# Performance work log

Hardware: AMD Instinct MI355X
Metric: run time of the kernel (lower is better)

The kernel has to match this reference:

```python
import jax, jax.numpy as jnp
import numpy as np

B_, L_, DM = 2, 2048, 1024
DS, DC, EXP, HD = 128, 4, 2, 64
DI = EXP * DM              # 2048
NH = DI // HD              # 32 heads
CONV_DIM = DI + 2 * DS     # 2304
DIN = 2 * DI + 2 * DS + NH # 4384 (z, xBC, dt)
CS = 256                   # SSD chunk size
EPS = 1e-5


def setup_inputs() -> dict:
    key = jax.random.key(0)
    ks = jax.random.split(key, 8)
    s = 0.02
    x = jax.random.normal(ks[0], (B_, L_, DM), jnp.float32)
    norm_w = jnp.ones((DM,), jnp.float32)
    in_proj_w = jax.random.normal(ks[1], (DIN, DM), jnp.float32) * s
    conv_w = jax.random.normal(ks[2], (CONV_DIM, DC), jnp.float32) * 0.2
    conv_b = jnp.zeros((CONV_DIM,), jnp.float32)
    # inverse-softplus of dt ~ U(0.001, 0.1)
    dt_bias = jnp.log(jnp.expm1(jax.random.uniform(ks[3], (NH,), minval=0.001, maxval=0.1)))
    A_log = jnp.log(jax.random.uniform(ks[4], (NH,), minval=1.0, maxval=16.0))
    D = jnp.ones((NH,), jnp.float32)
    gnorm_w = jnp.ones((DI,), jnp.float32)
    out_proj_w = jax.random.normal(ks[5], (DM, DI), jnp.float32) * s
    return dict(x=x, norm_w=norm_w, in_proj_w=in_proj_w, conv_w=conv_w, conv_b=conv_b,
                dt_bias=dt_bias, A_log=A_log, D=D, gnorm_w=gnorm_w, out_proj_w=out_proj_w)


def _segsum(a):
    # a: [..., T] -> [..., T, T]; (i,j) = sum_{j<k<=i} a_k, -inf above diagonal
    T = a.shape[-1]
    cs = jnp.cumsum(a, -1)
    seg = cs[..., :, None] - cs[..., None, :]
    mask = jnp.tril(jnp.ones((T, T), bool))
    return jnp.where(mask, seg, -jnp.inf)


def _ssd(X, A, Bm, Cm):
    # X: [b,l,h,p] (= x*dt), A: [b,l,h] (= dt*a), Bm,Cm: [b,l,n] (ngroups=1)
    b, l, h, p = X.shape
    n, nc = Bm.shape[-1], l // CS
    X = X.reshape(b, nc, CS, h, p)
    A = A.reshape(b, nc, CS, h).transpose(0, 3, 1, 2)  # [b,h,c,s]
    Bm = Bm.reshape(b, nc, CS, n)
    Cm = Cm.reshape(b, nc, CS, n)
    Acs = jnp.cumsum(A, -1)                            # [b,h,c,s]
    Lmat = jnp.exp(_segsum(A))                         # [b,h,c,s,s]
    Y_diag = jnp.einsum('bcln,bcsn,bhcls,bcshp->bclhp', Cm, Bm, Lmat, X)
    decay_states = jnp.exp(Acs[..., -1:] - Acs)        # [b,h,c,s]
    states = jnp.einsum('bcln,bhcl,bclhp->bchpn', Bm, decay_states, X)
    states = jnp.concatenate([jnp.zeros_like(states[:, :1]), states], axis=1)  # [b,c+1,h,p,n]
    decay_chunk = jnp.exp(_segsum(jnp.pad(Acs[..., -1], ((0, 0), (0, 0), (1, 0)))))  # [b,h,c+1,c+1]
    states = jnp.einsum('bhzc,bchpn->bzhpn', decay_chunk, states)[:, :-1]
    Y_off = jnp.einsum('bcln,bchpn,bhcl->bclhp', Cm, states, jnp.exp(Acs))
    return (Y_diag + Y_off).reshape(b, l, h, p)


def _forward(x, norm_w, in_proj_w, conv_w, conv_b, dt_bias, A_log, D, gnorm_w, out_proj_w):
    b, l, _ = x.shape
    # outer RMSNorm
    xn = x * jax.lax.rsqrt(jnp.mean(x * x, -1, keepdims=True) + EPS) * norm_w
    zxbcdt = jnp.einsum('bld,ed->ble', xn, in_proj_w)
    z = zxbcdt[..., :DI]
    xBC = zxbcdt[..., DI:DI + CONV_DIM]
    dt = zxbcdt[..., -NH:]
    # causal depthwise conv1d + bias + silu
    pad = jnp.pad(xBC, ((0, 0), (DC - 1, 0), (0, 0)))
    conv = sum(pad[:, k:k + l, :] * conv_w[:, k] for k in range(DC)) + conv_b
    xBC = conv * jax.nn.sigmoid(conv)
    xs = xBC[..., :DI]
    Bm = xBC[..., DI:DI + DS]
    Cm = xBC[..., DI + DS:]
    dt = jax.nn.softplus(dt + dt_bias)                 # [b,l,h]
    A = -jnp.exp(A_log)                                # [h]
    xh = xs.reshape(b, l, NH, HD)
    y = _ssd(xh * dt[..., None], dt * A, Bm, Cm)
    y = y + D[None, None, :, None] * xh
    y = y.reshape(b, l, DI)
    # gated RMSNorm (norm_before_gate=False): rmsnorm(y * silu(z)) * w
    y = y * (z * jax.nn.sigmoid(z))
    y = y * jax.lax.rsqrt(jnp.mean(y * y, -1, keepdims=True) + EPS) * gnorm_w
    return x + jnp.einsum('bld,ed->ble', y, out_proj_w)


def reference(x, norm_w, in_proj_w, conv_w, conv_b, dt_bias, A_log, D, gnorm_w, out_proj_w):
    return _forward(x, norm_w, in_proj_w, conv_w, conv_b, dt_bias, A_log, D, gnorm_w, out_proj_w)
```

## Files before the change

### kernel.cpp

```cpp
#include <hip/hip_runtime.h>
#include <hip/hip_bf16.h>

#define BB      2
#define LSEQ    2048
#define DMODEL  1024
#define DSTATE  128
#define DCONV   4
#define HEADDIM 64
#define DINNER  2048
#define NHEADS  32
#define CONVD   2304
#define DINP    4384
#define CHUNK   256
#define NCH     8
#define NROWS   4096
#define EPSF    1e-5f
#define TPAD    264
#define WIPAD   4480

typedef __attribute__((ext_vector_type(8))) short bf16x8;
typedef __attribute__((ext_vector_type(4))) float f32x4;

#define ASYNC_COPY16(gptr, lptr) \
    __builtin_amdgcn_global_load_lds((const __attribute__((address_space(1))) void*)(gptr), \
                                     (__attribute__((address_space(3))) void*)(lptr), 16, 0, 0)

__device__ __forceinline__ ushort f2bf(float f) {
    __hip_bfloat16 h = __float2bfloat16(f);
    return *(ushort*)&h;
}
__device__ __forceinline__ float bf2f(ushort u) {
    return __uint_as_float(((unsigned)u) << 16);
}
__device__ __forceinline__ short fb(float f) { return (short)f2bf(f); }
__device__ __forceinline__ short tb(float f) { return (short)(__float_as_uint(f) >> 16); }

__global__ __launch_bounds__(256) void prologue_kernel(
    const float* __restrict__ x, const float* __restrict__ norm_w,
    const float* __restrict__ in_proj_w, const float* __restrict__ out_proj_w,
    const float* __restrict__ gnorm_w,
    ushort* __restrict__ xn_bf, ushort* __restrict__ wi_bf,
    ushort* __restrict__ wo_bf, float* __restrict__ ssq)
{
    int bid = blockIdx.x;
    if (bid < 4480) {
        long i4 = ((long)bid * 256 + threadIdx.x) * 4;
        int n = (int)(i4 >> 10);
        long k = i4 & 1023;
        ushort4 o;
        if (n < DINP) {
            float4 v = *(const float4*)(in_proj_w + ((long)n << 10) + k);
            o.x = f2bf(v.x); o.y = f2bf(v.y); o.z = f2bf(v.z); o.w = f2bf(v.w);
        } else { o.x = o.y = o.z = o.w = 0; }
        *(ushort4*)(wi_bf + i4) = o;
    } else if (bid < 6528) {
        long i4 = ((long)(bid - 4480) * 256 + threadIdx.x) * 4;
        int k = (int)(i4 & 2047);
        float4 v = *(const float4*)(out_proj_w + i4);
        float4 g = *(const float4*)(gnorm_w + k);
        ushort4 o;
        o.x = f2bf(v.x * g.x); o.y = f2bf(v.y * g.y);
        o.z = f2bf(v.z * g.z); o.w = f2bf(v.w * g.w);
        *(ushort4*)(wo_bf + i4) = o;
    } else if (bid < 10624) {
        int row = bid - 6528;
        const float* xr = x + (long)row * DMODEL;
        float4 v = *(const float4*)(xr + threadIdx.x * 4);
        float ss = v.x*v.x + v.y*v.y + v.z*v.z + v.w*v.w;
        for (int off = 32; off; off >>= 1) ss += __shfl_down(ss, off, 64);
        __shared__ float red[4];
        if ((threadIdx.x & 63) == 0) red[threadIdx.x >> 6] = ss;
        __syncthreads();
        float tot = red[0] + red[1] + red[2] + red[3];
        float scale = rsqrtf(tot / (float)DMODEL + EPSF);
        float4 wv = *(const float4*)(norm_w + threadIdx.x * 4);
        ushort4 o;
        o.x = f2bf(v.x * scale * wv.x); o.y = f2bf(v.y * scale * wv.y);
        o.z = f2bf(v.z * scale * wv.z); o.w = f2bf(v.w * scale * wv.w);
        *(ushort4*)(xn_bf + (long)row * DMODEL + threadIdx.x * 4) = o;
    } else {
        ssq[(bid - 10624) * 256 + threadIdx.x] = 0.f;
    }
}

__global__ __launch_bounds__(256, 3) void gemm_bf16_kernel(
    const ushort* __restrict__ A, int lda, long sA,
    const ushort* __restrict__ W, int ldw, long sW,
    void* __restrict__ Cout, int ldc, long sC, int c_bf16,
    const float* __restrict__ resid, const float* __restrict__ rowscale,
    int mtiles, int ntiles, int N, int K)
{
    __shared__ __align__(16) char smem[34816];
    ushort* As = (ushort*)smem;
    ushort* Bs = As + 128 * 64;
    ushort* tu = (ushort*)smem;
    float*  tf = (float*)smem;

    const int t = threadIdx.x;
    const int lane = t & 63;
    const int w = t >> 6;
    const int wm = w & 1, wn = w >> 1;
    const int lm = lane & 15, quad = lane >> 4;

    int pid = blockIdx.x;
    const int GM = 8;
    int width = GM * ntiles;
    int group = pid / width;
    int first_m = group * GM;
    int gsz = mtiles - first_m; if (gsz > GM) gsz = GM;
    int mt = first_m + (pid % width) % gsz;
    int nt = (pid % width) / gsz;
    const int m0 = mt * 128, n0 = nt * 128;

    A += (long)blockIdx.z * sA;
    W += (long)blockIdx.z * sW;

    const ushort* ga[4]; const ushort* gw[4];
#pragma unroll
    for (int i = 0; i < 4; ++i) {
        int s = i * 256 + t;
        int row = s >> 3;
        int kseg = (s & 7) ^ (row & 7);
        ga[i] = A + (long)(m0 + row) * lda + kseg * 8;
        gw[i] = W + (long)(n0 + row) * ldw + kseg * 8;
    }

    f32x4 acc[4][4];
    f32x4 zero4 = {0.f, 0.f, 0.f, 0.f};
#pragma unroll
    for (int i = 0; i < 4; ++i)
#pragma unroll
        for (int j = 0; j < 4; ++j) acc[i][j] = zero4;

    int arow8[4], arow7[4], brow8[4], brow7[4];
#pragma unroll
    for (int i = 0; i < 4; ++i) {
        int ar = wm * 64 + i * 16 + lm;
        arow8[i] = ar * 8; arow7[i] = ar & 7;
        int br = wn * 64 + i * 16 + lm;
        brow8[i] = br * 8; brow7[i] = br & 7;
    }

    for (int k0 = 0; k0 < K; k0 += 64) {
#pragma unroll
        for (int i = 0; i < 4; ++i) {
            ASYNC_COPY16(ga[i], &As[(i * 256 + w * 64) * 8]);
            ga[i] += 64;
        }
#pragma unroll
        for (int i = 0; i < 4; ++i) {
            ASYNC_COPY16(gw[i], &Bs[(i * 256 + w * 64) * 8]);
            gw[i] += 64;
        }
        __syncthreads();
#pragma unroll
        for (int ks = 0; ks < 2; ++ks) {
            bf16x8 af[4], bfr[4];
#pragma unroll
            for (int i = 0; i < 4; ++i)
                af[i]  = *(const bf16x8*)&As[(arow8[i] + ((ks * 4 + quad) ^ arow7[i])) * 8];
#pragma unroll
            for (int i = 0; i < 4; ++i)
                bfr[i] = *(const bf16x8*)&Bs[(brow8[i] + ((ks * 4 + quad) ^ brow7[i])) * 8];
#pragma unroll
            for (int im = 0; im < 4; ++im)
#pragma unroll
                for (int in = 0; in < 4; ++in)
                    acc[im][in] = __builtin_amdgcn_mfma_f32_16x16x32_bf16(
                        af[im], bfr[in], acc[im][in], 0, 0, 0);
        }
        __syncthreads();
    }

    if (c_bf16) {
        ushort* C = (ushort*)Cout + (long)blockIdx.z * sC;
#pragma unroll
        for (int mi = 0; mi < 4; ++mi)
#pragma unroll
            for (int ni = 0; ni < 4; ++ni) {
                int c = wn * 64 + ni * 16 + lm;
#pragma unroll
                for (int i = 0; i < 4; ++i) {
                    int r = wm * 64 + mi * 16 + quad * 4 + i;
                    tu[r * 136 + c] = f2bf(acc[mi][ni][i]);
                }
            }
        __syncthreads();
        int r = t >> 1, cb = (t & 1) * 64;
        long rowbase = (long)(m0 + r) * ldc + n0 + cb;
#pragma unroll
        for (int q = 0; q < 8; ++q) {
            int gcol = n0 + cb + q * 8;
            if (gcol < N)
                *(bf16x8*)(C + rowbase + q * 8) =
                    *(const bf16x8*)&tu[r * 136 + cb + q * 8];
        }
    } else {
        float* C = (float*)Cout + (long)blockIdx.z * sC;
#pragma unroll
        for (int p = 0; p < 2; ++p) {
            if (wm == p) {
#pragma unroll
                for (int mi = 0; mi < 4; ++mi)
#pragma unroll
                    for (int i = 0; i < 4; ++i) {
                        int r = mi * 16 + quad * 4 + i;
                        float s = 1.f;
                        if (rowscale)
                            s = rsqrtf(rowscale[m0 + p * 64 + r] * (1.f / (float)DINNER) + EPSF);
#pragma unroll
                        for (int ni = 0; ni < 4; ++ni) {
                            int c = wn * 64 + ni * 16 + lm;
                            tf[r * 132 + c] = acc[mi][ni][i] * s;
                        }
                    }
            }
            __syncthreads();
            int r2 = t >> 2, cb = (t & 3) * 32;
            long gbase = (long)(m0 + p * 64 + r2) * ldc + n0 + cb;
#pragma unroll
            for (int q = 0; q < 8; ++q) {
                float4 v = *(const float4*)&tf[r2 * 132 + cb + q * 4];
                if (resid) {
                    float4 rv = *(const float4*)(resid + gbase + q * 4);
                    v.x += rv.x; v.y += rv.y; v.z += rv.z; v.w += rv.w;
                }
                *(float4*)(C + gbase + q * 4) = v;
            }
            __syncthreads();
        }
    }
}

__device__ __forceinline__ void conv8_row(
    const ushort* __restrict__ zx, const float* __restrict__ cw,
    const float* __restrict__ cb, ushort* __restrict__ xBC_bf,
    int row, int l, int c)
{
    float4 cwv[8];
#pragma unroll
    for (int j = 0; j < 8; ++j) cwv[j] = *(const float4*)(cw + (c + j) * 4);
    float acc[8];
    {
        float4 b0 = *(const float4*)(cb + c);
        float4 b1 = *(const float4*)(cb + c + 4);
        acc[0] = b0.x; acc[1] = b0.y; acc[2] = b0.z; acc[3] = b0.w;
        acc[4] = b1.x; acc[5] = b1.y; acc[6] = b1.z; acc[7] = b1.w;
    }
#pragma unroll
    for (int k = 0; k < DCONV; ++k) {
        int ls = l + k - (DCONV - 1);
        if (ls >= 0) {
            const ushort* zr = zx + (long)(row + k - (DCONV - 1)) * DINP + DINNER + c;
            ushort4 a = *(const ushort4*)zr;
            ushort4 b = *(const ushort4*)(zr + 4);
            acc[0] += bf2f(a.x) * ((const float*)&cwv[0])[k];
            acc[1] += bf2f(a.y) * ((const float*)&cwv[1])[k];
            acc[2] += bf2f(a.z) * ((const float*)&cwv[2])[k];
            acc[3] += bf2f(a.w) * ((const float*)&cwv[3])[k];
            acc[4] += bf2f(b.x) * ((const float*)&cwv[4])[k];
            acc[5] += bf2f(b.y) * ((const float*)&cwv[5])[k];
            acc[6] += bf2f(b.z) * ((const float*)&cwv[6])[k];
            acc[7] += bf2f(b.w) * ((const float*)&cwv[7])[k];
        }
    }
    ushort o[8];
#pragma unroll
    for (int j = 0; j < 8; ++j)
        o[j] = f2bf(acc[j] / (1.f + __expf(-acc[j])));
    ushort* dst = xBC_bf + (long)row * CONVD + c;
    *(ushort4*)dst = *(ushort4*)&o[0];
    *(ushort4*)(dst + 4) = *(ushort4*)&o[4];
}

__global__ __launch_bounds__(256) void conv_acs_kernel(
    const ushort* __restrict__ zx, const float* __restrict__ cw,
    const float* __restrict__ cb, ushort* __restrict__ xBC_bf,
    const float* __restrict__ dt_bias, const float* __restrict__ A_log,
    float* __restrict__ dtv, float* __restrict__ Acs)
{
    int bid = blockIdx.x;
    int t = threadIdx.x;
    if (bid < NROWS) {
        int row = bid;
        int l = row & (LSEQ - 1);
        conv8_row(zx, cw, cb, xBC_bf, row, l, t * 8);
        if (t < 32)
            conv8_row(zx, cw, cb, xBC_bf, row, l, 2048 + t * 8);
    } else {
        __shared__ float buf[2 * CHUNK];
        int idx = bid - NROWS;
        int bc = idx >> 5, h = idx & 31;
        int l = t;
        int row = bc * CHUNK + l;
        float v = bf2f(zx[(long)row * DINP + (DINP - NHEADS) + h]) + dt_bias[h];
        float d = (v > 20.f) ? v : log1pf(__expf(v));
        dtv[row * NHEADS + h] = d;
        float a = -d * __expf(A_log[h]);
        buf[l] = a; __syncthreads();
        int src = 0;
        for (int off = 1; off < CHUNK; off <<= 1) {
            float vv = buf[src * CHUNK + l];
            if (l >= off) vv += buf[src * CHUNK + l - off];
            buf[(src ^ 1) * CHUNK + l] = vv;
            __syncthreads();
            src ^= 1;
        }
        Acs[(bc * NHEADS + h) * CHUNK + l] = buf[src * CHUNK + l];
    }
}

__global__ __launch_bounds__(256) void prep_b_kernel(
    const ushort* __restrict__ xBC_bf, ushort* __restrict__ Bt)
{
    int bc = blockIdx.x, half = blockIdx.y;
    int t = threadIdx.x;
    int row0 = bc * CHUNK;
    __shared__ ushort tB[64 * TPAD];
    int src_c0 = DINNER + half * 64;
    for (int iter = 0; iter < 8; ++iter) {
        int l = iter * 32 + (t >> 3);
        int cc = (t & 7) * 8;
        ushort u[8];
        *(ushort4*)&u[0] = *(const ushort4*)(xBC_bf + (long)(row0 + l) * CONVD + src_c0 + cc);
        *(ushort4*)&u[4] = *(const ushort4*)(xBC_bf + (long)(row0 + l) * CONVD + src_c0 + cc + 4);
#pragma unroll
        for (int j = 0; j < 8; ++j) tB[(cc + j) * TPAD + l] = u[j];
    }
    __syncthreads();
    int r = t >> 2, seg = (t & 3) * 64;
    ushort* dst = Bt + ((long)bc * DSTATE + half * 64 + r) * CHUNK + seg;
    const ushort* s1 = &tB[r * TPAD + seg];
#pragma unroll
    for (int q = 0; q < 16; ++q)
        *(ushort4*)(dst + q * 4) = *(const ushort4*)(s1 + q * 4);
}

__global__ __launch_bounds__(256) void chunk_state_mfma_kernel(
    const ushort* __restrict__ xBC_bf, const ushort* __restrict__ Bt,
    const float* __restrict__ dtv, const float* __restrict__ acs,
    ushort* __restrict__ state)
{
    int bc = blockIdx.x, h = blockIdx.y;
    int t = threadIdx.x, lane = t & 63, w = t >> 6;
    int lm = lane & 15, quad = lane >> 4;
    int row0 = bc * CHUNK;
    __shared__ ushort xt[64 * TPAD];
    __shared__ float cl[CHUNK];
    {
        float a = acs[(bc * NHEADS + h) * CHUNK + t];
        float T = acs[(bc * NHEADS + h) * CHUNK + CHUNK - 1];
        cl[t] = __expf(T - a) * dtv[(row0 + t) * NHEADS + h];
    }
    __syncthreads();
    for (int iter = 0; iter < 8; ++iter) {
        int l = iter * 32 + (t >> 3);
        int cc = (t & 7) * 8;
        ushort u[8];
        *(ushort4*)&u[0] = *(const ushort4*)(xBC_bf + (long)(row0 + l) * CONVD + h * HEADDIM + cc);
        *(ushort4*)&u[4] = *(const ushort4*)(xBC_bf + (long)(row0 + l) * CONVD + h * HEADDIM + cc + 4);
        float sc = cl[l];
#pragma unroll
        for (int j = 0; j < 8; ++j)
            xt[(cc + j) * TPAD + l] = (ushort)tb(bf2f(u[j]) * sc);
    }
    __syncthreads();

    const ushort* Bb = Bt + (long)bc * DSTATE * CHUNK;
    f32x4 acc[4][2];
    f32x4 zero4 = {0.f, 0.f, 0.f, 0.f};
#pragma unroll
    for (int i = 0; i < 4; ++i) { acc[i][0] = zero4; acc[i][1] = zero4; }

    for (int kt = 0; kt < 8; ++kt) {
        int k = kt * 32 + quad * 8;
        bf16x8 af[4], bfr[2];
#pragma unroll
        for (int mi = 0; mi < 4; ++mi)
            af[mi] = *(const bf16x8*)&xt[(mi * 16 + lm) * TPAD + k];
#pragma unroll
        for (int nj = 0; nj < 2; ++nj)
            bfr[nj] = *(const bf16x8*)(Bb + (long)(w * 32 + nj * 16 + lm) * CHUNK + k);
#pragma unroll
        for (int mi = 0; mi < 4; ++mi)
#pragma unroll
            for (int nj = 0; nj < 2; ++nj)
                acc[mi][nj] = __builtin_amdgcn_mfma_f32_16x16x32_bf16(
                    af[mi], bfr[nj], acc[mi][nj], 0, 0, 0);
    }
    ushort* sp = state + (long)(bc * NHEADS + h) * (DSTATE * HEADDIM);
#pragma unroll
    for (int mi = 0; mi < 4; ++mi)
#pragma unroll
        for (int nj = 0; nj < 2; ++nj) {
            int n = w * 32 + nj * 16 + lm;
#pragma unroll
            for (int i = 0; i < 4; ++i) {
                int p = mi * 16 + quad * 4 + i;
                sp[p * DSTATE + n] = f2bf(acc[mi][nj][i]);
            }
        }
}

__global__ __launch_bounds__(256) void state_scan_kernel(
    ushort* __restrict__ state, const float* __restrict__ Acs)
{
    long flat = (long)blockIdx.x * 256 + threadIdx.x;
    int e = (int)(flat & 8191);
    int bh = (int)(flat >> 13);
    int b = bh >> 5, h = bh & 31;
    float S = 0.f;
    for (int c = 0; c < NCH; ++c) {
        int bc = b * NCH + c;
        long idx = ((long)(bc * NHEADS + h)) * 8192 + e;
        float T = Acs[(bc * NHEADS + h) * CHUNK + CHUNK - 1];
        float tmp = bf2f(state[idx]);
        state[idx] = f2bf(S);
        S = S * __expf(T) + tmp;
    }
}

__global__ __launch_bounds__(256) void ssd_y_mfma_kernel(
    const ushort* __restrict__ xBC_bf, const ushort* __restrict__ G2b,
    const float* __restrict__ acs, const ushort* __restrict__ state,
    const ushort* __restrict__ zxb, const float* __restrict__ dtv,
    const float* __restrict__ Dh, ushort* __restrict__ ybf,
    float* __restrict__ ssq)
{
    int bc = blockIdx.x, h = blockIdx.y;
    int t = threadIdx.x, lane = t & 63, w = t >> 6;
    int lm = lane & 15, quad = lane >> 4;
    int row0 = bc * CHUNK;
    __shared__ ushort xt[64 * TPAD];
    __shared__ float acs_s[CHUNK];
    __shared__ float dl[CHUNK];
    acs_s[t] = acs[(bc * NHEADS + h) * CHUNK + t];
    dl[t] = dtv[(row0 + t) * NHEADS + h];
    __syncthreads();
    for (int iter = 0; iter < 8; ++iter) {
        int l = iter * 32 + (t >> 3);
        int cc = (t & 7) * 8;
        ushort u[8];
        *(ushort4*)&u[0] = *(const ushort4*)(xBC_bf + (long)(row0 + l) * CONVD + h * HEADDIM + cc);
        *(ushort4*)&u[4] = *(const ushort4*)(xBC_bf + (long)(row0 + l) * CONVD + h * HEADDIM + cc + 4);
        float sd = dl[l];
#pragma unroll
        for (int j = 0; j < 8; ++j)
            xt[(cc + j) * TPAD + l] = (ushort)tb(bf2f(u[j]) * sd);
    }
    __syncthreads();

    int lbase = w * 64;
    float acs_l[4], eAl[4];
#pragma unroll
    for (int mi = 0; mi < 4; ++mi) {
        acs_l[mi] = acs_s[lbase + mi * 16 + lm];
        eAl[mi] = __expf(acs_l[mi]);
    }
    f32x4 acc[4][4];
    f32x4 zero4 = {0.f, 0.f, 0.f, 0.f};
#pragma unroll
    for (int i = 0; i < 4; ++i)
#pragma unroll
        for (int j = 0; j < 4; ++j) acc[i][j] = zero4;

    const ushort* g2 = G2b + (long)bc * (CHUNK * CHUNK);

    for (int ks = 0; ks <= 2 * w + 1; ++ks) {
        int sq = ks * 32 + quad * 8;
        bf16x8 bfr[4];
#pragma unroll
        for (int ni = 0; ni < 4; ++ni)
            bfr[ni] = *(const bf16x8*)&xt[(ni * 16 + lm) * TPAD + sq];
        float base = acs_s[sq];
        float e8[8];
        e8[0] = 1.f;
#pragma unroll
        for (int j = 1; j < 8; ++j)
            e8[j] = __expf(fminf(base - acs_s[sq + j], 80.f));
#pragma unroll
        for (int mi = 0; mi < 4; ++mi) {
            int lmin = lbase + mi * 16;
            if (ks * 32 > lmin + 15) continue;
            int lv = lmin + lm;
            float em = __expf(fminf(acs_l[mi] - base, 0.f));
            bf16x8 g8 = *(const bf16x8*)(g2 + (long)lv * CHUNK + sq);
            bf16x8 af;
#pragma unroll
            for (int j = 0; j < 8; ++j) {
                float v = bf2f((ushort)g8[j]) * (em * e8[j]);
                af[j] = (sq + j > lv) ? (short)0 : tb(v);
            }
#pragma unroll
            for (int ni = 0; ni < 4; ++ni)
                acc[mi][ni] = __builtin_amdgcn_mfma_f32_16x16x32_bf16(
                    af, bfr[ni], acc[mi][ni], 0, 0, 0);
        }
    }

    const ushort* sp = state + (long)(bc * NHEADS + h) * (DSTATE * HEADDIM);
    const ushort* Cb = xBC_bf + (long)row0 * CONVD + DINNER + DSTATE;
    for (int kt = 0; kt < 4; ++kt) {
        int n0 = kt * 32 + quad * 8;
        bf16x8 bfr[4];
#pragma unroll
        for (int ni = 0; ni < 4; ++ni)
            bfr[ni] = *(const bf16x8*)(sp + (long)(ni * 16 + lm) * DSTATE + n0);
#pragma unroll
        for (int mi = 0; mi < 4; ++mi) {
            int lv = lbase + mi * 16 + lm;
            bf16x8 cu = *(const bf16x8*)(Cb + (long)lv * CONVD + n0);
            bf16x8 ce;
            float e = eAl[mi];
#pragma unroll
            for (int j = 0; j < 8; ++j) ce[j] = tb(bf2f((ushort)cu[j]) * e);
#pragma unroll
            for (int ni = 0; ni < 4; ++ni)
                acc[mi][ni] = __builtin_amdgcn_mfma_f32_16x16x32_bf16(
                    ce, bfr[ni], acc[mi][ni], 0, 0, 0);
        }
    }

    float Dv = Dh[h];
#pragma unroll
    for (int mi = 0; mi < 4; ++mi)
#pragma unroll
        for (int i = 0; i < 4; ++i) {
            int l = lbase + mi * 16 + quad * 4 + i;
            long row = row0 + l;
            float ps = 0.f;
#pragma unroll
            for (int ni = 0; ni < 4; ++ni) {
                int p = ni * 16 + lm;
                float xh = bf2f(xBC_bf[row * CONVD + h * HEADDIM + p]);
                float z = bf2f(zxb[row * DINP + h * HEADDIM + p]);
                float o = (acc[mi][ni][i] + Dv * xh) * (z / (1.f + __expf(-z)));
                ps += o * o;
                ybf[row * DINNER + h * HEADDIM + p] = f2bf(o);
            }
#pragma unroll
            for (int m = 1; m < 16; m <<= 1) ps += __shfl_xor(ps, m, 64);
            if (lm == 0) atomicAdd(&ssq[row], ps);
        }
}

extern "C" void kernel_launch(void* const* d_in, const int* in_sizes, int n_in,
                              void* d_out, int out_size, void* d_ws, size_t ws_size,
                              hipStream_t stream)
{
    (void)in_sizes; (void)n_in; (void)out_size; (void)ws_size;
    const float* x          = (const float*)d_in[0];
    const float* norm_w     = (const float*)d_in[1];
    const float* in_proj_w  = (const float*)d_in[2];
    const float* conv_w     = (const float*)d_in[3];
    const float* conv_b     = (const float*)d_in[4];
    const float* dt_bias    = (const float*)d_in[5];
    const float* A_log      = (const float*)d_in[6];
    const float* Dh         = (const float*)d_in[7];
    const float* gnorm_w    = (const float*)d_in[8];
    const float* out_proj_w = (const float*)d_in[9];
    float* out = (float*)d_out;
    float* ws = (float*)d_ws;

    float* zxb_f   = ws;
    float* xbc_f   = zxb_f   + 8978432;
    float* dtv     = xbc_f   + 4718592;
    float* acs     = dtv     + 131072;
    float* g2_f    = acs     + 131072;
    float* state_f = g2_f    + 524288;
    float* bt_f    = state_f + 2097152;
    float* regU    = bt_f    + 262144;
    float* wo_f    = regU    + 4390912;
    float* ssq     = wo_f    + 1048576;

    ushort* zxb_bf = (ushort*)zxb_f;
    ushort* xBC_bf = (ushort*)xbc_f;
    ushort* G2b    = (ushort*)g2_f;
    ushort* state  = (ushort*)state_f;
    ushort* Bt     = (ushort*)bt_f;
    ushort* xn_bf  = (ushort*)regU;
    ushort* wi_bf  = (ushort*)(regU + 2097152);
    ushort* ybf    = (ushort*)regU;
    ushort* wo_bf  = (ushort*)wo_f;

    prologue_kernel<<<dim3(10640), 256, 0, stream>>>(
        x, norm_w, in_proj_w, out_proj_w, gnorm_w, xn_bf, wi_bf, wo_bf, ssq);

    gemm_bf16_kernel<<<dim3(32 * 35), 256, 0, stream>>>(
        xn_bf, DMODEL, 0, wi_bf, DMODEL, 0,
        zxb_bf, DINP, 0, 1, nullptr, nullptr, 32, 35, DINP, DMODEL);

    conv_acs_kernel<<<dim3(NROWS + BB * NCH * NHEADS), 256, 0, stream>>>(
        zxb_bf, conv_w, conv_b, xBC_bf, dt_bias, A_log, dtv, acs);

    prep_b_kernel<<<dim3(BB * NCH, 2), 256, 0, stream>>>(xBC_bf, Bt);

    gemm_bf16_kernel<<<dim3(4, 1, BB * NCH), 256, 0, stream>>>(
        xBC_bf + DINNER + DSTATE, CONVD, (long)CHUNK * CONVD,
        xBC_bf + DINNER, CONVD, (long)CHUNK * CONVD,
        G2b, CHUNK, (long)CHUNK * CHUNK, 1, nullptr, nullptr, 2, 2, CHUNK, DSTATE);

    chunk_state_mfma_kernel<<<dim3(BB * NCH, NHEADS), 256, 0, stream>>>(
        xBC_bf, Bt, dtv, acs, state);

    state_scan_kernel<<<dim3(BB * NHEADS * 8192 / 256), 256, 0, stream>>>(state, acs);

    ssd_y_mfma_kernel<<<dim3(BB * NCH, NHEADS), 256, 0, stream>>>(
        xBC_bf, G2b, acs, state, zxb_bf, dtv, Dh, ybf, ssq);

    gemm_bf16_kernel<<<dim3(32 * 8), 256, 0, stream>>>(
        ybf, DINNER, 0, wo_bf, DINNER, 0,
        out, DMODEL, 0, 0, x, ssq, 32, 8, DMODEL, DINNER);
}
```

Before: 300.0 us.

## Add XCD-aware block remap, 32-bit offsets, occupancy hint and narrow-tile Gram GEMM

The main GEMM kernel now remaps block IDs across the 8 XCDs so that neighbouring tiles land on the same die's L2. It keeps the global load offsets as 32-bit unsigned values to save registers, and raises the launch-bounds occupancy hint from 3 to 4. A new 128x64-tile GEMM variant with a smaller shared-memory footprint replaces the general kernel for the per-chunk C·B^T Gram matrix, doubling the block count there. Risks include register spills under the tighter launch bound and a remap that assumes the grid size is divisible by 8.

```diff
diff --git a/kernel.cpp b/kernel.cpp
--- a/kernel.cpp
+++ b/kernel.cpp
@@ -83,7 +83,7 @@
     }
 }
 
-__global__ __launch_bounds__(256, 3) void gemm_bf16_kernel(
+__global__ __launch_bounds__(256, 4) void gemm_bf16_kernel(
     const ushort* __restrict__ A, int lda, long sA,
     const ushort* __restrict__ W, int ldw, long sW,
     void* __restrict__ Cout, int ldc, long sC, int c_bf16,
@@ -102,7 +102,10 @@
     const int wm = w & 1, wn = w >> 1;
     const int lm = lane & 15, quad = lane >> 4;
 
-    int pid = blockIdx.x;
+    int nwg = gridDim.x;
+    int pid0 = blockIdx.x;
+    int pid = (pid0 & 7) * (nwg >> 3) + (pid0 >> 3);
+
     const int GM = 8;
     int width = GM * ntiles;
     int group = pid / width;
@@ -112,17 +115,17 @@
     int nt = (pid % width) / gsz;
     const int m0 = mt * 128, n0 = nt * 128;
 
-    A += (long)blockIdx.z * sA;
-    W += (long)blockIdx.z * sW;
-
-    const ushort* ga[4]; const ushort* gw[4];
+    const ushort* Ab = A + (long)blockIdx.z * sA;
+    const ushort* Wb = W + (long)blockIdx.z * sW;
+
+    unsigned ga[4], gw[4];
 #pragma unroll
     for (int i = 0; i < 4; ++i) {
         int s = i * 256 + t;
         int row = s >> 3;
         int kseg = (s & 7) ^ (row & 7);
-        ga[i] = A + (long)(m0 + row) * lda + kseg * 8;
-        gw[i] = W + (long)(n0 + row) * ldw + kseg * 8;
+        ga[i] = (unsigned)((m0 + row) * lda + kseg * 8);
+        gw[i] = (unsigned)((n0 + row) * ldw + kseg * 8);
     }
 
     f32x4 acc[4][4];
@@ -144,12 +147,12 @@
     for (int k0 = 0; k0 < K; k0 += 64) {
 #pragma unroll
         for (int i = 0; i < 4; ++i) {
-            ASYNC_COPY16(ga[i], &As[(i * 256 + w * 64) * 8]);
+            ASYNC_COPY16(Ab + ga[i], &As[(i * 256 + w * 64) * 8]);
             ga[i] += 64;
         }
 #pragma unroll
         for (int i = 0; i < 4; ++i) {
-            ASYNC_COPY16(gw[i], &Bs[(i * 256 + w * 64) * 8]);
+            ASYNC_COPY16(Wb + gw[i], &Bs[(i * 256 + w * 64) * 8]);
             gw[i] += 64;
         }
         __syncthreads();
@@ -229,6 +232,119 @@
             }
             __syncthreads();
         }
+    }
+}
+
+__global__ __launch_bounds__(256, 4) void gemm_bf16_s_kernel(
+    const ushort* __restrict__ A, int lda, long sA,
+    const ushort* __restrict__ W, int ldw, long sW,
+    ushort* __restrict__ Cout, int ldc, long sC,
+    int mtiles, int ntiles, int N, int K)
+{
+    __shared__ __align__(16) char smem[24576];
+    ushort* As = (ushort*)smem;
+    ushort* Bs = As + 128 * 64;
+    ushort* tu = (ushort*)smem;
+
+    const int t = threadIdx.x;
+    const int lane = t & 63;
+    const int w = t >> 6;
+    const int wm = w & 1, wn = w >> 1;
+    const int lm = lane & 15, quad = lane >> 4;
+
+    int pid = blockIdx.x;
+    int mt = pid % mtiles;
+    int nt = pid / mtiles;
+    const int m0 = mt * 128, n0 = nt * 64;
+
+    A += (long)blockIdx.z * sA;
+    W += (long)blockIdx.z * sW;
+
+    const ushort* ga[4]; const ushort* gw[2];
+#pragma unroll
+    for (int i = 0; i < 4; ++i) {
+        int s = i * 256 + t;
+        int row = s >> 3;
+        int kseg = (s & 7) ^ (row & 7);
+        ga[i] = A + (long)(m0 + row) * lda + kseg * 8;
+    }
+#pragma unroll
+    for (int i = 0; i < 2; ++i) {
+        int s = i * 256 + t;
+        int row = s >> 3;
+        int kseg = (s & 7) ^ (row & 7);
+        gw[i] = W + (long)(n0 + row) * ldw + kseg * 8;
+    }
+
+    f32x4 acc[4][2];
+    f32x4 zero4 = {0.f, 0.f, 0.f, 0.f};
+#pragma unroll
+    for (int i = 0; i < 4; ++i) { acc[i][0] = zero4; acc[i][1] = zero4; }
+
+    int arow8[4], arow7[4], brow8[2], brow7[2];
+#pragma unroll
+    for (int i = 0; i < 4; ++i) {
+        int ar = wm * 64 + i * 16 + lm;
+        arow8[i] = ar * 8; arow7[i] = ar & 7;
+    }
+#pragma unroll
+    for (int i = 0; i < 2; ++i) {
+        int br = wn * 32 + i * 16 + lm;
+        brow8[i] = br * 8; brow7[i] = br & 7;
+    }
+
+    for (int k0 = 0; k0 < K; k0 += 64) {
+#pragma unroll
+        for (int i = 0; i < 4; ++i) {
+            ASYNC_COPY16(ga[i], &As[(i * 256 + w * 64) * 8]);
+            ga[i] += 64;
+        }
+#pragma unroll
+        for (int i = 0; i < 2; ++i) {
+            ASYNC_COPY16(gw[i], &Bs[(i * 256 + w * 64) * 8]);
+            gw[i] += 64;
+        }
+        __syncthreads();
+#pragma unroll
+        for (int ks = 0; ks < 2; ++ks) {
+            bf16x8 af[4], bfr[2];
+#pragma unroll
+            for (int i = 0; i < 4; ++i)
+                af[i]  = *(const bf16x8*)&As[(arow8[i] + ((ks * 4 + quad) ^ arow7[i])) * 8];
+#pragma unroll
+            for (int i = 0; i < 2; ++i)
+                bfr[i] = *(const bf16x8*)&Bs[(brow8[i] + ((ks * 4 + quad) ^ brow7[i])) * 8];
+#pragma unroll
+            for (int im = 0; im < 4; ++im)
+#pragma unroll
+                for (int in = 0; in < 2; ++in)
+                    acc[im][in] = __builtin_amdgcn_mfma_f32_16x16x32_bf16(
+                        af[im], bfr[in], acc[im][in], 0, 0, 0);
+        }
+        __syncthreads();
+    }
+
+    ushort* C = Cout + (long)blockIdx.z * sC;
+#pragma unroll
+    for (int mi = 0; mi < 4; ++mi)
+#pragma unroll
+        for (int ni = 0; ni < 2; ++ni) {
+            int c = wn * 32 + ni * 16 + lm;
+#pragma unroll
+            for (int i = 0; i < 4; ++i) {
+                int r = wm * 64 + mi * 16 + quad * 4 + i;
+                tu[r * 72 + c] = f2bf(acc[mi][ni][i]);
+            }
+        }
+    __syncthreads();
+    int r = t >> 1, cb = (t & 1) * 32;
+    long rowbase = (long)(m0 + r) * ldc + n0 + cb;
+#pragma unroll
+    for (int q = 0; q < 4; ++q) {
+        int gcol = n0 + cb + q * 8;
+        if (gcol < N)
+            *(bf16x8*)(C + rowbase + q * 8) =
+                *(const bf16x8*)&tu[r * 72 + cb + q * 8];
     }
 }
 
@@ -595,10 +711,10 @@
 
     prep_b_kernel<<<dim3(BB * NCH, 2), 256, 0, stream>>>(xBC_bf, Bt);
 
-    gemm_bf16_kernel<<<dim3(4, 1, BB * NCH), 256, 0, stream>>>(
+    gemm_bf16_s_kernel<<<dim3(8, 1, BB * NCH), 256, 0, stream>>>(
         xBC_bf + DINNER + DSTATE, CONVD, (long)CHUNK * CONVD,
         xBC_bf + DINNER, CONVD, (long)CHUNK * CONVD,
-        G2b, CHUNK, (long)CHUNK * CHUNK, 1, nullptr, nullptr, 2, 2, CHUNK, DSTATE);
+        G2b, CHUNK, (long)CHUNK * CHUNK, 2, 4, CHUNK, DSTATE);
 
     chunk_state_mfma_kernel<<<dim3(BB * NCH, NHEADS), 256, 0, stream>>>(
         xBC_bf, Bt, dtv, acs, state);
```

After: 318.2 us. +6.1%, slower.
